# Kernel tuning notes

Hardware: AMD Instinct MI355X
Metric: run time of the kernel (lower is better)

The kernel has to match this reference:

```python
import jax, jax.numpy as jnp
import numpy as np

DIM = 2048
N_HEADS = 32
N_KV_HEADS = 8
HEAD_DIM = DIM // N_HEADS


def setup_inputs() -> dict:
    key = jax.random.key(0)
    ks = jax.random.split(key, 5)
    B, N = 2, 2048
    s = 1.0 / np.sqrt(DIM)
    x = jax.random.normal(ks[0], (B, N, DIM), dtype=jnp.float32)
    wq = jax.random.normal(ks[1], (DIM, N_HEADS * HEAD_DIM), dtype=jnp.float32) * s
    wk = jax.random.normal(ks[2], (DIM, N_KV_HEADS * HEAD_DIM), dtype=jnp.float32) * s
    wv = jax.random.normal(ks[3], (DIM, N_KV_HEADS * HEAD_DIM), dtype=jnp.float32) * s
    wo = jax.random.normal(ks[4], (N_HEADS * HEAD_DIM, DIM), dtype=jnp.float32) * s
    return {"x": x, "wq": wq, "wk": wk, "wv": wv, "wo": wo}


def reference(x, wq, wk, wv, wo):
    B, N, D = x.shape
    H, KVH, Hd = N_HEADS, N_KV_HEADS, HEAD_DIM
    rep = H // KVH
    # projections -> [B, heads, N, Hd]
    q = (x @ wq).reshape(B, N, H, Hd).transpose(0, 2, 1, 3)
    k = (x @ wk).reshape(B, N, KVH, Hd).transpose(0, 2, 1, 3)
    v = (x @ wv).reshape(B, N, KVH, Hd).transpose(0, 2, 1, 3)
    if KVH < H:
        k = jnp.repeat(k, rep, axis=1)  # repeat_interleave on head dim
        v = jnp.repeat(v, rep, axis=1)
    scale = 1.0 / np.sqrt(Hd).astype(np.float32)
    attn = jnp.einsum('bhnd,bhmd->bhnm', q, k) * scale  # [B,H,N,N]
    attn = jax.nn.softmax(attn, axis=-1)
    out = jnp.einsum('bhnm,bhmd->bhnd', attn, v)
    out = out.transpose(0, 2, 1, 3).reshape(B, N, H * Hd)
    return out @ wo
```

## Files before the change

### kernel.cpp

```cpp
#include <hip/hip_runtime.h>

typedef unsigned short u16;
typedef __attribute__((ext_vector_type(8))) short bh8;
typedef __attribute__((ext_vector_type(4))) float f4;

__device__ inline u16 f2bf(float f) {
  union { float f; unsigned u; } v; v.f = f;
  unsigned r = v.u + 0x7FFFu + ((v.u >> 16) & 1u);
  return (u16)(r >> 16);
}

__global__ __launch_bounds__(256) void convx_kernel(const float* __restrict__ x,
                                                    u16* __restrict__ xb, int n8) {
  int i = blockIdx.x * 256 + threadIdx.x;
  if (i >= n8) return;
  const float4* xf = (const float4*)x;
  float4 a = xf[2 * i], b = xf[2 * i + 1];
  alignas(16) u16 o[8] = { f2bf(a.x), f2bf(a.y), f2bf(a.z), f2bf(a.w),
                           f2bf(b.x), f2bf(b.y), f2bf(b.z), f2bf(b.w) };
  *(int4*)(xb + (size_t)i * 8) = *(const int4*)o;
}

__global__ __launch_bounds__(256) void tconv_kernel(const float* __restrict__ W,
                                                    u16* __restrict__ Wt,
                                                    int K, int N) {
  __shared__ float tile[32][33];
  int nb = blockIdx.x * 32, kb = blockIdx.y * 32;
  int tx = threadIdx.x, ty = threadIdx.y;
  for (int i = ty; i < 32; i += 8)
    tile[i][tx] = W[(size_t)(kb + i) * N + nb + tx];
  __syncthreads();
  for (int i = ty; i < 32; i += 8)
    Wt[(size_t)(nb + i) * K + kb + tx] = f2bf(tile[tx][i]);
}

__global__ __launch_bounds__(256) void vtrans_kernel(const u16* __restrict__ QKV,
                                                     u16* __restrict__ VT) {
  __shared__ u16 tile[32][33];
  int nb = blockIdx.x * 32, cb = blockIdx.y * 32, b = blockIdx.z;
  int tx = threadIdx.x, ty = threadIdx.y;
  for (int i = ty; i < 32; i += 8)
    tile[i][tx] = QKV[(size_t)(b * 2048 + nb + i) * 3072 + 2560 + cb + tx];
  __syncthreads();
  for (int i = ty; i < 32; i += 8)
    VT[((size_t)b * 512 + cb + i) * 2048 + nb + tx] = tile[tx][i];
}

__device__ inline void gload16(const u16* g, u16* l) {
  __builtin_amdgcn_global_load_lds(
      (const __attribute__((address_space(1))) unsigned int*)g,
      (__attribute__((address_space(3))) unsigned int*)l, 16, 0, 0);
}

__device__ inline unsigned cvtpk_bf16(float lo, float hi) {
  unsigned r;
  asm("v_cvt_pk_bf16_f32 %0, %1, %2" : "=v"(r) : "v"(lo), "v"(hi));
  return r;
}

#define QK_SC2 0.18033688011112042f

template <typename OutT, bool SCALEQ = false>
__global__ __launch_bounds__(256) void gemm_bt(const u16* __restrict__ A,
                                               const u16* __restrict__ Bt,
                                               OutT* __restrict__ C,
                                               int M, int N, int K) {
  __shared__ u16 As[128 * 32];
  __shared__ u16 Bs[128 * 32];
  const int t = threadIdx.x;
  const int lane = t & 63, w = t >> 6;
  const int wr = w >> 1, wc = w & 1;
  const int fr = lane & 15, fq = lane >> 4;
  const int rowBase = blockIdx.y * 128, colBase = blockIdx.x * 128;
  f4 acc[4][4] = {};
  const u16* Ag = A + (size_t)rowBase * K;
  const u16* Bg = Bt + (size_t)colBase * K;
  for (int kt = 0; kt < K; kt += 32) {
    __syncthreads();
#pragma unroll
    for (int i = 0; i < 2; i++) {
      int c = t + i * 256;
      gload16(Ag + (size_t)(c >> 2) * K + kt + (c & 3) * 8, As + c * 8);
    }
#pragma unroll
    for (int i = 0; i < 2; i++) {
      int c = t + i * 256;
      gload16(Bg + (size_t)(c >> 2) * K + kt + (c & 3) * 8, Bs + c * 8);
    }
    __syncthreads();
    bh8 a[4], b[4];
#pragma unroll
    for (int m = 0; m < 4; m++)
      a[m] = *(const bh8*)(As + (wr * 64 + m * 16 + fr) * 32 + fq * 8);
#pragma unroll
    for (int n = 0; n < 4; n++)
      b[n] = *(const bh8*)(Bs + (wc * 64 + n * 16 + fr) * 32 + fq * 8);
#pragma unroll
    for (int m = 0; m < 4; m++)
#pragma unroll
      for (int n = 0; n < 4; n++)
        acc[m][n] = __builtin_amdgcn_mfma_f32_16x16x32_bf16(a[m], b[n], acc[m][n], 0, 0, 0);
  }
#pragma unroll
  for (int m = 0; m < 4; m++)
#pragma unroll
    for (int n = 0; n < 4; n++)
#pragma unroll
      for (int r = 0; r < 4; r++) {
        int row = rowBase + wr * 64 + m * 16 + fq * 4 + r;
        int col = colBase + wc * 64 + n * 16 + fr;
        float v = acc[m][n][r];
        if constexpr (SCALEQ) {
          if (col < 2048) v *= QK_SC2;
        }
        if constexpr (sizeof(OutT) == 2)
          ((u16*)C)[(size_t)row * N + col] = f2bf(v);
        else
          ((float*)C)[(size_t)row * N + col] = v;
      }
}

__global__ __launch_bounds__(256) void attn_kernel(const u16* __restrict__ QKV,
                                                   const u16* __restrict__ VT,
                                                   u16* __restrict__ AO) {
  __shared__ u16 Ks[2][4096];
  __shared__ u16 Vs[2][4096];
  __shared__ u16 Plds[4][16][64];
  const int t = threadIdx.x, lane = t & 63, w = t >> 6;
  const int fr = lane & 15, fq = lane >> 4;
  const int blk = blockIdx.x;
  const int qt = blk & 15;
  const int h  = (blk >> 4) & 31;
  const int b  = blk >> 9;
  const int kvh = h >> 2;
  const size_t rowb = (size_t)b * 2048;
  const u16* Qb  = QKV + rowb * 3072 + h * 64;
  const u16* Kb  = QKV + rowb * 3072 + 2048 + kvh * 64;
  const u16* VTb = VT + ((size_t)b * 512 + kvh * 64) * 2048;
  const int qrow0 = qt * 128 + w * 32;

  bh8 qf[2][2];
#pragma unroll
  for (int sub = 0; sub < 2; sub++)
#pragma unroll
    for (int kk = 0; kk < 2; kk++)
      qf[sub][kk] = *(const bh8*)(Qb + (size_t)(qrow0 + sub * 16 + fr) * 3072 + kk * 32 + fq * 8);

  const bh8 ones8 = {0x3F80, 0x3F80, 0x3F80, 0x3F80, 0x3F80, 0x3F80, 0x3F80, 0x3F80};

  const int c0 = t, c1 = t + 256;
  const int r0 = c0 >> 3, s0 = (c0 ^ r0) & 7;
  const int r1 = c1 >> 3, s1 = (c1 ^ r1) & 7;
  const u16* ksrc0 = Kb  + (size_t)r0 * 3072 + s0 * 8;
  const u16* ksrc1 = Kb  + (size_t)r1 * 3072 + s1 * 8;
  const u16* vsrc0 = VTb + (size_t)r0 * 2048 + s0 * 8;
  const u16* vsrc1 = VTb + (size_t)r1 * 2048 + s1 * 8;

#define STAGE(buf, kb_) do {                                              \
    gload16(ksrc0 + (size_t)(kb_) * 64 * 3072, &Ks[buf][c0 * 8]);         \
    gload16(ksrc1 + (size_t)(kb_) * 64 * 3072, &Ks[buf][c1 * 8]);         \
    gload16(vsrc0 + (size_t)(kb_) * 64,        &Vs[buf][c0 * 8]);         \
    gload16(vsrc1 + (size_t)(kb_) * 64,        &Vs[buf][c1 * 8]);         \
  } while (0)

  STAGE(0, 0);
  asm volatile("s_waitcnt vmcnt(0)");
  __syncthreads();

  const unsigned rdOf = (unsigned)(fr * 128) + ((unsigned)(fq ^ (fr & 7)) << 4);
  char* Prow = (char*)&Plds[w][fr][0];
  const unsigned pswz = (unsigned)((fr & 7) << 4);

  f4 oacc[2][4] = {};
  f4 lacc[2] = {};

  for (int kb = 0; kb < 32; kb++) {
    const int cur = kb & 1;
    if (kb + 1 < 32) STAGE(cur ^ 1, kb + 1);

    const char* Kt  = (const char*)&Ks[cur][0];
    const char* Vtl = (const char*)&Vs[cur][0];

    f4 sf[2][4];
#pragma unroll
    for (int c = 0; c < 4; c++) {
      bh8 k0 = *(const bh8*)(Kt + c * 2048 + rdOf);
      bh8 k1 = *(const bh8*)(Kt + c * 2048 + (rdOf ^ 64));
      f4 s0v = {}, s1v = {};
      s0v = __builtin_amdgcn_mfma_f32_16x16x32_bf16(k0, qf[0][0], s0v, 0, 0, 0);
      s0v = __builtin_amdgcn_mfma_f32_16x16x32_bf16(k1, qf[0][1], s0v, 0, 0, 0);
      s1v = __builtin_amdgcn_mfma_f32_16x16x32_bf16(k0, qf[1][0], s1v, 0, 0, 0);
      s1v = __builtin_amdgcn_mfma_f32_16x16x32_bf16(k1, qf[1][1], s1v, 0, 0, 0);
      sf[0][c] = s0v; sf[1][c] = s1v;
    }

    bh8 pa[2][2];
#pragma unroll
    for (int sub = 0; sub < 2; sub++) {
#pragma unroll
      for (int c = 0; c < 4; c++) {
        float p0 = exp2f(sf[sub][c][0]);
        float p1 = exp2f(sf[sub][c][1]);
        float p2 = exp2f(sf[sub][c][2]);
        float p3 = exp2f(sf[sub][c][3]);
        union { unsigned u[2]; unsigned long long ll; } pk;
        pk.u[0] = cvtpk_bf16(p0, p1);
        pk.u[1] = cvtpk_bf16(p2, p3);
        *(unsigned long long*)(Prow + (((unsigned)(c * 32 + fq * 8)) ^ pswz)) = pk.ll;
      }
      pa[sub][0] = *(const bh8*)(Prow + (((unsigned)(fq * 16)) ^ pswz));
      pa[sub][1] = *(const bh8*)(Prow + (((unsigned)(64 + fq * 16)) ^ pswz));
      asm volatile("s_waitcnt lgkmcnt(0)" ::: "memory");
    }

#pragma unroll
    for (int hc = 0; hc < 4; hc++) {
      bh8 v0 = *(const bh8*)(Vtl + hc * 2048 + rdOf);
      bh8 v1 = *(const bh8*)(Vtl + hc * 2048 + (rdOf ^ 64));
      oacc[0][hc] = __builtin_amdgcn_mfma_f32_16x16x32_bf16(pa[0][0], v0, oacc[0][hc], 0, 0, 0);
      oacc[0][hc] = __builtin_amdgcn_mfma_f32_16x16x32_bf16(pa[0][1], v1, oacc[0][hc], 0, 0, 0);
      oacc[1][hc] = __builtin_amdgcn_mfma_f32_16x16x32_bf16(pa[1][0], v0, oacc[1][hc], 0, 0, 0);
      oacc[1][hc] = __builtin_amdgcn_mfma_f32_16x16x32_bf16(pa[1][1], v1, oacc[1][hc], 0, 0, 0);
    }
    lacc[0] = __builtin_amdgcn_mfma_f32_16x16x32_bf16(pa[0][0], ones8, lacc[0], 0, 0, 0);
    lacc[0] = __builtin_amdgcn_mfma_f32_16x16x32_bf16(pa[0][1], ones8, lacc[0], 0, 0, 0);
    lacc[1] = __builtin_amdgcn_mfma_f32_16x16x32_bf16(pa[1][0], ones8, lacc[1], 0, 0, 0);
    lacc[1] = __builtin_amdgcn_mfma_f32_16x16x32_bf16(pa[1][1], ones8, lacc[1], 0, 0, 0);

    asm volatile("s_waitcnt vmcnt(0)");
    __syncthreads();
  }
#undef STAGE

#pragma unroll
  for (int sub = 0; sub < 2; sub++)
#pragma unroll
    for (int r = 0; r < 4; r++) {
      float inv = 1.f / lacc[sub][r];
#pragma unroll
      for (int hc = 0; hc < 4; hc++) {
        float v = oacc[sub][hc][r] * inv;
        AO[(rowb + qrow0 + sub * 16 + fq * 4 + r) * 2048 + h * 64 + hc * 16 + fr] = f2bf(v);
      }
    }
}

extern "C" void kernel_launch(void* const* d_in, const int* in_sizes, int n_in,
                              void* d_out, int out_size, void* d_ws, size_t ws_size,
                              hipStream_t stream) {
  const float* x  = (const float*)d_in[0];
  const float* wq = (const float*)d_in[1];
  const float* wk = (const float*)d_in[2];
  const float* wv = (const float*)d_in[3];
  const float* wo = (const float*)d_in[4];
  float* out = (float*)d_out;
  char* ws = (char*)d_ws;
  u16* xb    = (u16*)(ws);
  u16* AO    = (u16*)(ws);
  u16* wqkvT = (u16*)(ws + 16777216);
  u16* VT    = (u16*)(ws + 16777216);
  u16* woT   = (u16*)(ws + 16777216 + 12582912);
  u16* QKV   = (u16*)(ws + 37748736);

  convx_kernel<<<4096, 256, 0, stream>>>(x, xb, 1048576);
  dim3 tb(32, 8);
  tconv_kernel<<<dim3(64, 64), tb, 0, stream>>>(wq, wqkvT, 2048, 2048);
  tconv_kernel<<<dim3(16, 64), tb, 0, stream>>>(wk, wqkvT + (size_t)2048 * 2048, 2048, 512);
  tconv_kernel<<<dim3(16, 64), tb, 0, stream>>>(wv, wqkvT + (size_t)2560 * 2048, 2048, 512);
  tconv_kernel<<<dim3(64, 64), tb, 0, stream>>>(wo, woT, 2048, 2048);

  gemm_bt<u16, true><<<dim3(24, 32), 256, 0, stream>>>(xb, wqkvT, QKV, 4096, 3072, 2048);
  vtrans_kernel<<<dim3(64, 16, 2), tb, 0, stream>>>(QKV, VT);
  attn_kernel<<<1024, 256, 0, stream>>>(QKV, VT, AO);
  gemm_bt<float><<<dim3(16, 32), 256, 0, stream>>>(AO, woT, out, 4096, 2048, 2048);
}
```

Before: 275.9 us.

## Deepen GEMM K-tile to 64 with XOR-swizzled LDS and fold Q scale into weights

The GEMM now stages a 64-wide K slice per iteration, which halves the number of barrier-separated load rounds. The LDS layout is XOR-swizzled so the 16-byte fragment reads avoid bank conflicts. The softmax scale for Q moves from the GEMM epilogue into the weight transpose-conversion. This changes rounding slightly, because Wq is scaled before the bf16 conversion, and doubles the LDS per block.

```diff
diff --git a/kernel.cpp b/kernel.cpp
--- a/kernel.cpp
+++ b/kernel.cpp
@@ -23,7 +23,7 @@
 
 __global__ __launch_bounds__(256) void tconv_kernel(const float* __restrict__ W,
                                                     u16* __restrict__ Wt,
-                                                    int K, int N) {
+                                                    int K, int N, float scale) {
   __shared__ float tile[32][33];
   int nb = blockIdx.x * 32, kb = blockIdx.y * 32;
   int tx = threadIdx.x, ty = threadIdx.y;
@@ -31,7 +31,7 @@
     tile[i][tx] = W[(size_t)(kb + i) * N + nb + tx];
   __syncthreads();
   for (int i = ty; i < 32; i += 8)
-    Wt[(size_t)(nb + i) * K + kb + tx] = f2bf(tile[tx][i]);
+    Wt[(size_t)(nb + i) * K + kb + tx] = f2bf(tile[tx][i] * scale);
 }
 
 __global__ __launch_bounds__(256) void vtrans_kernel(const u16* __restrict__ QKV,
@@ -60,13 +60,13 @@
 
 #define QK_SC2 0.18033688011112042f
 
-template <typename OutT, bool SCALEQ = false>
+template <typename OutT>
 __global__ __launch_bounds__(256) void gemm_bt(const u16* __restrict__ A,
                                                const u16* __restrict__ Bt,
                                                OutT* __restrict__ C,
                                                int M, int N, int K) {
-  __shared__ u16 As[128 * 32];
-  __shared__ u16 Bs[128 * 32];
+  __shared__ u16 As[128 * 64];
+  __shared__ u16 Bs[128 * 64];
   const int t = threadIdx.x;
   const int lane = t & 63, w = t >> 6;
   const int wr = w >> 1, wc = w & 1;
@@ -75,31 +75,42 @@
   f4 acc[4][4] = {};
   const u16* Ag = A + (size_t)rowBase * K;
   const u16* Bg = Bt + (size_t)colBase * K;
-  for (int kt = 0; kt < K; kt += 32) {
+  for (int kt = 0; kt < K; kt += 64) {
     __syncthreads();
 #pragma unroll
-    for (int i = 0; i < 2; i++) {
+    for (int i = 0; i < 4; i++) {
       int c = t + i * 256;
-      gload16(Ag + (size_t)(c >> 2) * K + kt + (c & 3) * 8, As + c * 8);
-    }
-#pragma unroll
-    for (int i = 0; i < 2; i++) {
+      int row = c >> 3, sl = (c ^ row) & 7;
+      gload16(Ag + (size_t)row * K + kt + sl * 8, As + c * 8);
+    }
+#pragma unroll
+    for (int i = 0; i < 4; i++) {
       int c = t + i * 256;
-      gload16(Bg + (size_t)(c >> 2) * K + kt + (c & 3) * 8, Bs + c * 8);
+      int row = c >> 3, sl = (c ^ row) & 7;
+      gload16(Bg + (size_t)row * K + kt + sl * 8, Bs + c * 8);
     }
     __syncthreads();
-    bh8 a[4], b[4];
-#pragma unroll
-    for (int m = 0; m < 4; m++)
-      a[m] = *(const bh8*)(As + (wr * 64 + m * 16 + fr) * 32 + fq * 8);
-#pragma unroll
-    for (int n = 0; n < 4; n++)
-      b[n] = *(const bh8*)(Bs + (wc * 64 + n * 16 + fr) * 32 + fq * 8);
-#pragma unroll
-    for (int m = 0; m < 4; m++)
-#pragma unroll
-      for (int n = 0; n < 4; n++)
-        acc[m][n] = __builtin_amdgcn_mfma_f32_16x16x32_bf16(a[m], b[n], acc[m][n], 0, 0, 0);
+#pragma unroll
+    for (int kk = 0; kk < 2; kk++) {
+      bh8 a[4], b[4];
+#pragma unroll
+      for (int m = 0; m < 4; m++) {
+        int row = wr * 64 + m * 16 + fr;
+        int sl = (kk * 4 + fq) ^ (row & 7);
+        a[m] = *(const bh8*)(As + row * 64 + sl * 8);
+      }
+#pragma unroll
+      for (int n = 0; n < 4; n++) {
+        int row = wc * 64 + n * 16 + fr;
+        int sl = (kk * 4 + fq) ^ (row & 7);
+        b[n] = *(const bh8*)(Bs + row * 64 + sl * 8);
+      }
+#pragma unroll
+      for (int m = 0; m < 4; m++)
+#pragma unroll
+        for (int n = 0; n < 4; n++)
+          acc[m][n] = __builtin_amdgcn_mfma_f32_16x16x32_bf16(a[m], b[n], acc[m][n], 0, 0, 0);
+    }
   }
 #pragma unroll
   for (int m = 0; m < 4; m++)
@@ -110,9 +121,6 @@
         int row = rowBase + wr * 64 + m * 16 + fq * 4 + r;
         int col = colBase + wc * 64 + n * 16 + fr;
         float v = acc[m][n][r];
-        if constexpr (SCALEQ) {
-          if (col < 2048) v *= QK_SC2;
-        }
         if constexpr (sizeof(OutT) == 2)
           ((u16*)C)[(size_t)row * N + col] = f2bf(v);
         else
@@ -264,12 +272,12 @@
 
   convx_kernel<<<4096, 256, 0, stream>>>(x, xb, 1048576);
   dim3 tb(32, 8);
-  tconv_kernel<<<dim3(64, 64), tb, 0, stream>>>(wq, wqkvT, 2048, 2048);
-  tconv_kernel<<<dim3(16, 64), tb, 0, stream>>>(wk, wqkvT + (size_t)2048 * 2048, 2048, 512);
-  tconv_kernel<<<dim3(16, 64), tb, 0, stream>>>(wv, wqkvT + (size_t)2560 * 2048, 2048, 512);
-  tconv_kernel<<<dim3(64, 64), tb, 0, stream>>>(wo, woT, 2048, 2048);
-
-  gemm_bt<u16, true><<<dim3(24, 32), 256, 0, stream>>>(xb, wqkvT, QKV, 4096, 3072, 2048);
+  tconv_kernel<<<dim3(64, 64), tb, 0, stream>>>(wq, wqkvT, 2048, 2048, QK_SC2);
+  tconv_kernel<<<dim3(16, 64), tb, 0, stream>>>(wk, wqkvT + (size_t)2048 * 2048, 2048, 512, 1.0f);
+  tconv_kernel<<<dim3(16, 64), tb, 0, stream>>>(wv, wqkvT + (size_t)2560 * 2048, 2048, 512, 1.0f);
+  tconv_kernel<<<dim3(64, 64), tb, 0, stream>>>(wo, woT, 2048, 2048, 1.0f);
+
+  gemm_bt<u16><<<dim3(24, 32), 256, 0, stream>>>(xb, wqkvT, QKV, 4096, 3072, 2048);
   vtrans_kernel<<<dim3(64, 16, 2), tb, 0, stream>>>(QKV, VT);
   attn_kernel<<<1024, 256, 0, stream>>>(QKV, VT, AO);
   gemm_bt<float><<<dim3(16, 32), 256, 0, stream>>>(AO, woT, out, 4096, 2048, 2048);
```

Result: faster. 253.0 us (-8.3%).
